# Kernel tuning notes

Hardware: AMD Instinct MI355X
Metric: run time of the kernel (lower is better)

Reference implementation:

```python
import jax, jax.numpy as jnp
import numpy as np

B, M, N, K = 256, 512, 512, 128
ALPHA = 0.0025  # a_scale * b_scale (per-tensor dequant factor)


def setup_inputs() -> dict:
    key = jax.random.key(0)
    k1, k2 = jax.random.split(key)
    # int8 quantized activations; 'a' row-major [B, M, K], 'b' stored as [B, N, K]
    a = jax.random.randint(k1, (B, M, K), -128, 128, dtype=jnp.int8)
    b = jax.random.randint(k2, (B, N, K), -128, 128, dtype=jnp.int8)
    alpha = jnp.float32(ALPHA)
    return {"a": a, "b": b, "alpha": alpha}


def reference(a, b, alpha):
    # with fused per-tensor scale dequant to fp32 in the epilogue.
    # out[b, m, n] = alpha * sum_k a[b, m, k] * b[b, n, k]
    acc = jnp.einsum(
        "bmk,bnk->bmn",
        a.astype(jnp.int32),
        b.astype(jnp.int32),
    )  # [B, M, N] int32 accumulator
    return acc.astype(jnp.float32) * alpha
```

## Files before the change

kernel.cpp:

```cpp
#include <hip/hip_runtime.h>
#include <stdint.h>

#define BATCH 256
#define M 512
#define N 512
#define K 128

typedef int int4v __attribute__((ext_vector_type(4)));

__global__ __launch_bounds__(512, 2) void bmm_s8s8_f32_kernel(
    const int* __restrict__ A32,
    const int* __restrict__ B32,
    const float* __restrict__ alpha_p,
    float* __restrict__ O)
{
    __shared__ int8_t As[M * K];
    __shared__ int8_t Bs[N * K];

    const int tid = threadIdx.x;
    const int bat = blockIdx.x;

    const int* Ag = A32 + (size_t)bat * (M * K);
    const int* Bg = B32 + (size_t)bat * (N * K);

#pragma unroll 4
    for (int i = 0; i < 32; ++i) {
        const int g   = i * 512 + tid;
        const int row = g >> 5;
        const int kg  = g & 31;
        const int kc  = kg >> 2;
        const int sub = kg & 3;
        const int kcs = kc ^ (row & 7);

        int4v wa = *(const int4v*)(Ag + (size_t)g * 4);
        int4v wb = *(const int4v*)(Bg + (size_t)g * 4);
        const int pa = (wa.x & 0xff) | ((wa.y & 0xff) << 8) |
                       ((wa.z & 0xff) << 16) | (wa.w << 24);
        const int pb = (wb.x & 0xff) | ((wb.y & 0xff) << 8) |
                       ((wb.z & 0xff) << 16) | (wb.w << 24);
        *(int*)(As + row * 128 + kcs * 16 + sub * 4) = pa;
        *(int*)(Bs + row * 128 + kcs * 16 + sub * 4) = pb;
    }
    __syncthreads();

    const int lane = tid & 63;
    const int wave = tid >> 6;
    const int l15  = lane & 15;
    const int quad = lane >> 4;
    const int sn   = wave;

    int4v bf[2][4];
#pragma unroll
    for (int ks = 0; ks < 2; ++ks)
#pragma unroll
        for (int j = 0; j < 4; ++j) {
            const int rb = sn * 64 + j * 16 + l15;
            const int kc = (ks * 4 + quad) ^ (rb & 7);
            bf[ks][j] = *(const int4v*)(Bs + rb * 128 + kc * 16);
        }

    const float alpha = *alpha_p;

    for (int sm = 0; sm < 8; ++sm) {
        int4v af[2][4];
#pragma unroll
        for (int ks = 0; ks < 2; ++ks)
#pragma unroll
            for (int i = 0; i < 4; ++i) {
                const int ra = sm * 64 + i * 16 + l15;
                const int kc = (ks * 4 + quad) ^ (ra & 7);
                af[ks][i] = *(const int4v*)(As + ra * 128 + kc * 16);
            }

        int4v acc[4][4];
#pragma unroll
        for (int i = 0; i < 4; ++i)
#pragma unroll
            for (int j = 0; j < 4; ++j)
                acc[i][j] = (int4v){0, 0, 0, 0};

#pragma unroll
        for (int ks = 0; ks < 2; ++ks)
#pragma unroll
            for (int i = 0; i < 4; ++i)
#pragma unroll
                for (int j = 0; j < 4; ++j)
                    acc[i][j] = __builtin_amdgcn_mfma_i32_16x16x64_i8(
                        af[ks][i], bf[ks][j], acc[i][j], 0, 0, 0);

        float* Ob = O + ((size_t)bat * M + sm * 64 + quad * 4) * N + sn * 64 + l15;
#pragma unroll
        for (int i = 0; i < 4; ++i)
#pragma unroll
            for (int r = 0; r < 4; ++r) {
                float* rowp = Ob + (size_t)(i * 16 + r) * N;
#pragma unroll
                for (int j = 0; j < 4; ++j)
                    rowp[j * 16] = alpha * (float)acc[i][j][r];
            }
    }
}

extern "C" void kernel_launch(void* const* d_in, const int* in_sizes, int n_in,
                              void* d_out, int out_size, void* d_ws, size_t ws_size,
                              hipStream_t stream) {
    const int*   a     = (const int*)d_in[0];
    const int*   b     = (const int*)d_in[1];
    const float* alpha = (const float*)d_in[2];
    float*       out   = (float*)d_out;

    dim3 grid(BATCH);
    dim3 block(512);
    bmm_s8s8_f32_kernel<<<grid, block, 0, stream>>>(a, b, alpha, out);
}
```

Measured before the change: 361.6 us.

## Swap MFMA operands to emit vectorized nontemporal float4 output stores

Swaps the A and B operands of the MFMA so each lane's four accumulator values fall along N instead of M. That lets the epilogue write a contiguous float4 per lane with a nontemporal store, where before it issued scattered scalar stores. The accumulation is also reordered to finish each 16x16 tile and store it right away, which lowers register pressure. The goal is to cut store instruction count and improve write coalescing on the large fp32 output, at the cost of less interleaving between independent MFMAs.

```diff
diff --git a/kernel.cpp b/kernel.cpp
--- a/kernel.cpp
+++ b/kernel.cpp
@@ -7,6 +7,7 @@
 #define K 128
 
 typedef int int4v __attribute__((ext_vector_type(4)));
+typedef float float4v __attribute__((ext_vector_type(4)));
 
 __global__ __launch_bounds__(512, 2) void bmm_s8s8_f32_kernel(
     const int* __restrict__ A32,
@@ -72,32 +73,25 @@
                 af[ks][i] = *(const int4v*)(As + ra * 128 + kc * 16);
             }
 
-        int4v acc[4][4];
+        float* Obase = O + ((size_t)bat * M + sm * 64 + l15) * N + sn * 64 + quad * 4;
 #pragma unroll
-        for (int i = 0; i < 4; ++i)
+        for (int i = 0; i < 4; ++i) {
 #pragma unroll
-            for (int j = 0; j < 4; ++j)
-                acc[i][j] = (int4v){0, 0, 0, 0};
-
+            for (int j = 0; j < 4; ++j) {
+                int4v acc = (int4v){0, 0, 0, 0};
 #pragma unroll
-        for (int ks = 0; ks < 2; ++ks)
-#pragma unroll
-            for (int i = 0; i < 4; ++i)
-#pragma unroll
-                for (int j = 0; j < 4; ++j)
-                    acc[i][j] = __builtin_amdgcn_mfma_i32_16x16x64_i8(
-                        af[ks][i], bf[ks][j], acc[i][j], 0, 0, 0);
-
-        float* Ob = O + ((size_t)bat * M + sm * 64 + quad * 4) * N + sn * 64 + l15;
-#pragma unroll
-        for (int i = 0; i < 4; ++i)
-#pragma unroll
-            for (int r = 0; r < 4; ++r) {
-                float* rowp = Ob + (size_t)(i * 16 + r) * N;
-#pragma unroll
-                for (int j = 0; j < 4; ++j)
-                    rowp[j * 16] = alpha * (float)acc[i][j][r];
+                for (int ks = 0; ks < 2; ++ks)
+                    acc = __builtin_amdgcn_mfma_i32_16x16x64_i8(
+                        bf[ks][j], af[ks][i], acc, 0, 0, 0);
+                float4v v;
+                v.x = alpha * (float)acc.x;
+                v.y = alpha * (float)acc.y;
+                v.z = alpha * (float)acc.z;
+                v.w = alpha * (float)acc.w;
+                __builtin_nontemporal_store(
+                    v, (float4v*)(Obase + (size_t)(i * 16) * N + j * 16));
             }
+        }
     }
 }
 
```

After: 397.6 us. 1.1x slower.

## Split each batch into 2x2 output tiles with swizzled block mapping

Applied to the files above, without the earlier changes.

Each batch is now handled by four blocks, each covering a 256x256 output quadrant, so shared memory per block drops from 128KB to 64KB and launch bounds allow more resident blocks. Blocks are remapped so that the four tiles of a batch are spread across XCD-interleaved block IDs. Global loads are batched four at a time before packing, to raise memory-level parallelism. The cost is that each A and B row block is read twice from global memory.

```diff
diff --git a/kernel.cpp b/kernel.cpp
--- a/kernel.cpp
+++ b/kernel.cpp
@@ -6,40 +6,53 @@
 #define N 512
 #define K 128
 
+
 typedef int int4v __attribute__((ext_vector_type(4)));
 
-__global__ __launch_bounds__(512, 2) void bmm_s8s8_f32_kernel(
+__global__ __launch_bounds__(512, 4) void bmm_s8s8_f32_kernel(
     const int* __restrict__ A32,
     const int* __restrict__ B32,
     const float* __restrict__ alpha_p,
     float* __restrict__ O)
 {
-    __shared__ int8_t As[M * K];
-    __shared__ int8_t Bs[N * K];
+    __shared__ int8_t As[256 * K];
+    __shared__ int8_t Bs[256 * K];
 
     const int tid = threadIdx.x;
-    const int bat = blockIdx.x;
 
-    const int* Ag = A32 + (size_t)bat * (M * K);
-    const int* Bg = B32 + (size_t)bat * (N * K);
+    const int bid  = (int)blockIdx.x;
+    const int vbid = (bid & 7) * 128 + (bid >> 3);
+    const int bat  = vbid >> 2;
+    const int mt   = (vbid >> 1) & 1;
+    const int nt   = vbid & 1;
 
-#pragma unroll 4
-    for (int i = 0; i < 32; ++i) {
-        const int g   = i * 512 + tid;
-        const int row = g >> 5;
-        const int kg  = g & 31;
-        const int kc  = kg >> 2;
-        const int sub = kg & 3;
-        const int kcs = kc ^ (row & 7);
+    const int* Ag = A32 + (size_t)bat * (M * K) + (size_t)mt * 256 * K;
+    const int* Bg = B32 + (size_t)bat * (N * K) + (size_t)nt * 256 * K;
 
-        int4v wa = *(const int4v*)(Ag + (size_t)g * 4);
-        int4v wb = *(const int4v*)(Bg + (size_t)g * 4);
-        const int pa = (wa.x & 0xff) | ((wa.y & 0xff) << 8) |
-                       ((wa.z & 0xff) << 16) | (wa.w << 24);
-        const int pb = (wb.x & 0xff) | ((wb.y & 0xff) << 8) |
-                       ((wb.z & 0xff) << 16) | (wb.w << 24);
-        *(int*)(As + row * 128 + kcs * 16 + sub * 4) = pa;
-        *(int*)(Bs + row * 128 + kcs * 16 + sub * 4) = pb;
+#pragma unroll
+    for (int ob = 0; ob < 4; ++ob) {
+        int4v wa[4], wb[4];
+#pragma unroll
+        for (int u = 0; u < 4; ++u) {
+            const int g = (ob * 4 + u) * 512 + tid;
+            wa[u] = *(const int4v*)(Ag + (size_t)g * 4);
+            wb[u] = *(const int4v*)(Bg + (size_t)g * 4);
+        }
+#pragma unroll
+        for (int u = 0; u < 4; ++u) {
+            const int g   = (ob * 4 + u) * 512 + tid;
+            const int row = g >> 5;
+            const int kg  = g & 31;
+            const int kc  = kg >> 2;
+            const int sub = kg & 3;
+            const int kcs = kc ^ (row & 7);
+            const int pa = (wa[u].x & 0xff) | ((wa[u].y & 0xff) << 8) |
+                           ((wa[u].z & 0xff) << 16) | (wa[u].w << 24);
+            const int pb = (wb[u].x & 0xff) | ((wb[u].y & 0xff) << 8) |
+                           ((wb[u].z & 0xff) << 16) | (wb[u].w << 24);
+            *(int*)(As + row * 128 + kcs * 16 + sub * 4) = pa;
+            *(int*)(Bs + row * 128 + kcs * 16 + sub * 4) = pb;
+        }
     }
     __syncthreads();
 
@@ -47,21 +60,20 @@
     const int wave = tid >> 6;
     const int l15  = lane & 15;
     const int quad = lane >> 4;
-    const int sn   = wave;
 
-    int4v bf[2][4];
+    int4v bf[2][2];
 #pragma unroll
     for (int ks = 0; ks < 2; ++ks)
 #pragma unroll
-        for (int j = 0; j < 4; ++j) {
-            const int rb = sn * 64 + j * 16 + l15;
+        for (int j = 0; j < 2; ++j) {
+            const int rb = wave * 32 + j * 16 + l15;
             const int kc = (ks * 4 + quad) ^ (rb & 7);
             bf[ks][j] = *(const int4v*)(Bs + rb * 128 + kc * 16);
         }
 
     const float alpha = *alpha_p;
 
-    for (int sm = 0; sm < 8; ++sm) {
+    for (int sm = 0; sm < 4; ++sm) {
         int4v af[2][4];
 #pragma unroll
         for (int ks = 0; ks < 2; ++ks)
@@ -72,11 +84,11 @@
                 af[ks][i] = *(const int4v*)(As + ra * 128 + kc * 16);
             }
 
-        int4v acc[4][4];
+        int4v acc[4][2];
 #pragma unroll
         for (int i = 0; i < 4; ++i)
 #pragma unroll
-            for (int j = 0; j < 4; ++j)
+            for (int j = 0; j < 2; ++j)
                 acc[i][j] = (int4v){0, 0, 0, 0};
 
 #pragma unroll
@@ -84,18 +96,19 @@
 #pragma unroll
             for (int i = 0; i < 4; ++i)
 #pragma unroll
-                for (int j = 0; j < 4; ++j)
+                for (int j = 0; j < 2; ++j)
                     acc[i][j] = __builtin_amdgcn_mfma_i32_16x16x64_i8(
                         af[ks][i], bf[ks][j], acc[i][j], 0, 0, 0);
 
-        float* Ob = O + ((size_t)bat * M + sm * 64 + quad * 4) * N + sn * 64 + l15;
+        float* Ob = O + ((size_t)bat * M + mt * 256 + sm * 64 + quad * 4) * N +
+                    nt * 256 + wave * 32 + l15;
 #pragma unroll
         for (int i = 0; i < 4; ++i)
 #pragma unroll
             for (int r = 0; r < 4; ++r) {
                 float* rowp = Ob + (size_t)(i * 16 + r) * N;
 #pragma unroll
-                for (int j = 0; j < 4; ++j)
+                for (int j = 0; j < 2; ++j)
                     rowp[j * 16] = alpha * (float)acc[i][j][r];
             }
     }
@@ -109,7 +122,7 @@
     const float* alpha = (const float*)d_in[2];
     float*       out   = (float*)d_out;
 
-    dim3 grid(BATCH);
+    dim3 grid(BATCH * 4);
     dim3 block(512);
     bmm_s8s8_f32_kernel<<<grid, block, 0, stream>>>(a, b, alpha, out);
 }
```

Measured after the change: 379.4 us. 1.05x slower.

## Stream A tiles per m-block to overlap global loads with MFMA compute

Applied to the files above, without the earlier changes.

Instead of loading all of A into LDS before any compute, the kernel now loads only the first 64-row A slab up front along with all of B. It prefetches the next slab into registers during each m-block iteration and writes it to LDS after the epilogue stores, with a barrier. This aims to hide global load latency behind MFMA and output stores. It adds per-iteration barriers and extra register pressure. Interleaving A loads with output stores also contends for memory bandwidth.

```diff
diff --git a/kernel.cpp b/kernel.cpp
--- a/kernel.cpp
+++ b/kernel.cpp
@@ -23,6 +23,14 @@
     const int* Ag = A32 + (size_t)bat * (M * K);
     const int* Bg = B32 + (size_t)bat * (N * K);
 
+
+    int4v a0[4];
+#pragma unroll
+    for (int u = 0; u < 4; ++u) {
+        const int g = u * 512 + tid;
+        a0[u] = *(const int4v*)(Ag + (size_t)g * 4);
+    }
+
 #pragma unroll 4
     for (int i = 0; i < 32; ++i) {
         const int g   = i * 512 + tid;
@@ -31,15 +39,23 @@
         const int kc  = kg >> 2;
         const int sub = kg & 3;
         const int kcs = kc ^ (row & 7);
-
-        int4v wa = *(const int4v*)(Ag + (size_t)g * 4);
         int4v wb = *(const int4v*)(Bg + (size_t)g * 4);
-        const int pa = (wa.x & 0xff) | ((wa.y & 0xff) << 8) |
-                       ((wa.z & 0xff) << 16) | (wa.w << 24);
         const int pb = (wb.x & 0xff) | ((wb.y & 0xff) << 8) |
                        ((wb.z & 0xff) << 16) | (wb.w << 24);
+        *(int*)(Bs + row * 128 + kcs * 16 + sub * 4) = pb;
+    }
+
+#pragma unroll
+    for (int u = 0; u < 4; ++u) {
+        const int g   = u * 512 + tid;
+        const int row = g >> 5;
+        const int kg  = g & 31;
+        const int kc  = kg >> 2;
+        const int sub = kg & 3;
+        const int kcs = kc ^ (row & 7);
+        const int pa = (a0[u].x & 0xff) | ((a0[u].y & 0xff) << 8) |
+                       ((a0[u].z & 0xff) << 16) | (a0[u].w << 24);
         *(int*)(As + row * 128 + kcs * 16 + sub * 4) = pa;
-        *(int*)(Bs + row * 128 + kcs * 16 + sub * 4) = pb;
     }
     __syncthreads();
 
@@ -62,6 +78,15 @@
     const float alpha = *alpha_p;
 
     for (int sm = 0; sm < 8; ++sm) {
+        int4v pre[4];
+        if (sm < 7) {
+#pragma unroll
+            for (int u = 0; u < 4; ++u) {
+                const int g = (sm + 1) * 2048 + u * 512 + tid;
+                pre[u] = *(const int4v*)(Ag + (size_t)g * 4);
+            }
+        }
+
         int4v af[2][4];
 #pragma unroll
         for (int ks = 0; ks < 2; ++ks)
@@ -98,6 +123,24 @@
                 for (int j = 0; j < 4; ++j)
                     rowp[j * 16] = alpha * (float)acc[i][j][r];
             }
+
+        if (sm < 7) {
+#pragma unroll
+            for (int u = 0; u < 4; ++u) {
+                const int g   = (sm + 1) * 2048 + u * 512 + tid;
+                const int row = g >> 5;
+                const int kg  = g & 31;
+                const int kc  = kg >> 2;
+                const int sub = kg & 3;
+                const int kcs = kc ^ (row & 7);
+                const int pa = (pre[u].x & 0xff) | ((pre[u].y & 0xff) << 8) |
+                               ((pre[u].z & 0xff) << 16) | (pre[u].w << 24);
+                *(int*)(As + row * 128 + kcs * 16 + sub * 4) = pa;
+            }
+            asm volatile("s_waitcnt lgkmcnt(0)" ::: "memory");
+            __builtin_amdgcn_s_barrier();
+            __builtin_amdgcn_sched_barrier(0);
+        }
     }
 }
 
```

Result: no change. 360.4 us (-0.3%).
